# Performance work log

Measured on AMD Instinct MI355X. Metric: run time of the kernel, lower is better.

The kernel has to match this reference:

```python
import jax, jax.numpy as jnp
import numpy as np

CAP = 6.0
EPS = 1e-5

def _layernorm(x, g, b):
    mu = jnp.mean(x, axis=-1, keepdims=True)
    var = jnp.mean(jnp.square(x - mu), axis=-1, keepdims=True)
    return (x - mu) * jax.lax.rsqrt(var + EPS) * g + b

def setup_inputs() -> dict:
    key = jax.random.key(0)
    B, S, D, H = 4, 1024, 1024, 16
    DF = int(D * 2.0)
    ks = jax.random.split(key, 8)
    inp = {
        "x": jax.random.normal(ks[0], (B, S, D), dtype=jnp.float32),
        "mask": jnp.tril(jnp.ones((S, S), dtype=bool)),  # causal block mask
        "qkv_w": jax.random.normal(ks[1], (3 * D, D), dtype=jnp.float32) * 0.02,
        "qkv_b": jnp.zeros((3 * D,), dtype=jnp.float32),
        "out_w": jax.random.normal(ks[2], (D, D), dtype=jnp.float32) * 0.02,
        "out_b": jnp.zeros((D,), dtype=jnp.float32),
        "ln1_g": jnp.ones((D,), dtype=jnp.float32),
        "ln1_b": jnp.zeros((D,), dtype=jnp.float32),
        "ln2_g": jnp.ones((D,), dtype=jnp.float32),
        "ln2_b": jnp.zeros((D,), dtype=jnp.float32),
        "ff1_w": jax.random.normal(ks[3], (DF, D), dtype=jnp.float32) * 0.02,
        "ff1_b": jnp.zeros((DF,), dtype=jnp.float32),
        "ff2_w": jax.random.normal(ks[4], (D, DF), dtype=jnp.float32) * 0.02,
        "ff2_b": jnp.zeros((D,), dtype=jnp.float32),
    }
    return inp

def reference(x, mask, qkv_w, qkv_b, out_w, out_b, ln1_g, ln1_b, ln2_g, ln2_b,
              ff1_w, ff1_b, ff2_w, ff2_b):
    B, S, D = x.shape
    H = 16
    dh = D // H
    res = x
    h = _layernorm(x, ln1_g, ln1_b)
    qkv = h @ qkv_w.T + qkv_b                       # [B,S,3D]
    qkv = qkv.reshape(B, S, 3, H, dh).transpose(2, 0, 3, 1, 4)  # [3,B,H,S,dh]
    q, k, v = qkv[0], qkv[1], qkv[2]
    scores = jnp.einsum('bhqd,bhkd->bhqk', q, k) / jnp.sqrt(jnp.float32(dh))
    scores = CAP * jnp.tanh(scores / CAP)            # logit soft-cap score_mod
    scores = jnp.where(mask, scores, jnp.float32(-1e9))
    attn = jax.nn.softmax(scores, axis=-1)
    o = jnp.einsum('bhqk,bhkd->bhqd', attn, v)       # [B,H,S,dh]
    o = o.transpose(0, 2, 1, 3).reshape(B, S, D)
    x = res + (o @ out_w.T + out_b)
    h2 = _layernorm(x, ln2_g, ln2_b)
    ff = jax.nn.gelu(h2 @ ff1_w.T + ff1_b, approximate=False) @ ff2_w.T + ff2_b
    return x + ff
```

## Files before the change

kernel.cpp:

```cpp
#include <hip/hip_runtime.h>
#include <hip/hip_bf16.h>
#include <cmath>

#define NROWS 4096
#define DM    1024

typedef unsigned short u16;
typedef __attribute__((ext_vector_type(8))) short short8;
typedef __attribute__((ext_vector_type(4))) float floatx4;

#if __has_builtin(__builtin_amdgcn_exp2f)
#define EXP2F(x) __builtin_amdgcn_exp2f(x)
#else
#define EXP2F(x) exp2f(x)
#endif
#if __has_builtin(__builtin_amdgcn_rcpf)
#define RCPF(x) __builtin_amdgcn_rcpf(x)
#else
#define RCPF(x) (1.0f / (x))
#endif

__device__ __forceinline__ u16 f2bf(float f) {
    unsigned int u = __float_as_uint(f);
    return (u16)((u + 0x7fffu + ((u >> 16) & 1u)) >> 16);
}

__device__ __forceinline__ size_t pk_off(int row, int k, int KB) {
    const int rt = row >> 6, i = (row >> 4) & 3, lr = row & 15;
    const int kb = k >> 6, s = (k >> 5) & 1, lq = (k >> 3) & 3, j = k & 7;
    return ((((size_t)(rt * KB + kb) * 2 + s) * 4 + i) * 64 + lq * 16 + lr) * 8 + j;
}

__device__ __forceinline__ void async_copy16(const void* g, void* l) {
    __builtin_amdgcn_global_load_lds(
        (const __attribute__((address_space(1))) void*)g,
        (__attribute__((address_space(3))) void*)l, 16, 0, 0);
}

__global__ __launch_bounds__(256) void castln_kernel(
    const float* __restrict__ s0, const float* __restrict__ s1,
    const float* __restrict__ s2, const float* __restrict__ s3,
    u16* __restrict__ d0, u16* __restrict__ d1,
    u16* __restrict__ d2, u16* __restrict__ d3,
    const float* __restrict__ x, const float* __restrict__ g,
    const float* __restrict__ beta, u16* __restrict__ hout)
{
    const int bid = blockIdx.x;
    if (bid < 8192) {
        const float* s; u16* d; int base, kbits, KB;
        if (bid < 3072)      { s = s0; d = d0; base = bid;        kbits = 10; KB = 16; }
        else if (bid < 4096) { s = s1; d = d1; base = bid - 3072; kbits = 10; KB = 16; }
        else if (bid < 6144) { s = s2; d = d2; base = bid - 4096; kbits = 10; KB = 16; }
        else                 { s = s3; d = d3; base = bid - 6144; kbits = 11; KB = 32; }
        const int idx = (base * 256 + threadIdx.x) * 4;
        const float4 v = *(const float4*)(s + idx);
        const int row = idx >> kbits, k = idx & ((1 << kbits) - 1);
        *(ushort4*)(d + pk_off(row, k, KB)) =
            make_ushort4(f2bf(v.x), f2bf(v.y), f2bf(v.z), f2bf(v.w));
        return;
    }
    const int row = bid - 8192;
    const int t = threadIdx.x;
    const float4 v = ((const float4*)(x + (size_t)row * DM))[t];
    float s = v.x + v.y + v.z + v.w;
    #pragma unroll
    for (int off = 32; off > 0; off >>= 1) s += __shfl_xor(s, off);
    __shared__ float red[4];
    const int wid = t >> 6;
    if ((t & 63) == 0) red[wid] = s;
    __syncthreads();
    const float mean = (red[0] + red[1] + red[2] + red[3]) * (1.0f / DM);
    const float dx = v.x - mean, dy = v.y - mean, dz = v.z - mean, dw = v.w - mean;
    float ss = dx*dx + dy*dy + dz*dz + dw*dw;
    #pragma unroll
    for (int off = 32; off > 0; off >>= 1) ss += __shfl_xor(ss, off);
    __syncthreads();
    if ((t & 63) == 0) red[wid] = ss;
    __syncthreads();
    const float var = (red[0] + red[1] + red[2] + red[3]) * (1.0f / DM);
    const float rstd = rsqrtf(var + 1e-5f);
    const float4 gv = ((const float4*)g)[t];
    const float4 bv = ((const float4*)beta)[t];
    *(ushort4*)(hout + pk_off(row, t * 4, 16)) = make_ushort4(
        f2bf(dx * rstd * gv.x + bv.x), f2bf(dy * rstd * gv.y + bv.y),
        f2bf(dz * rstd * gv.z + bv.z), f2bf(dw * rstd * gv.w + bv.w));
}

__global__ __launch_bounds__(256) void ln_kernel(
    const float* __restrict__ x, const float* __restrict__ g,
    const float* __restrict__ beta, u16* __restrict__ out)
{
    const int row = blockIdx.x;
    const int t = threadIdx.x;
    const float4 v = ((const float4*)(x + (size_t)row * DM))[t];
    float s = v.x + v.y + v.z + v.w;
    #pragma unroll
    for (int off = 32; off > 0; off >>= 1) s += __shfl_xor(s, off);
    __shared__ float red[4];
    const int wid = t >> 6;
    if ((t & 63) == 0) red[wid] = s;
    __syncthreads();
    const float mean = (red[0] + red[1] + red[2] + red[3]) * (1.0f / DM);
    const float dx = v.x - mean, dy = v.y - mean, dz = v.z - mean, dw = v.w - mean;
    float ss = dx*dx + dy*dy + dz*dz + dw*dw;
    #pragma unroll
    for (int off = 32; off > 0; off >>= 1) ss += __shfl_xor(ss, off);
    __syncthreads();
    if ((t & 63) == 0) red[wid] = ss;
    __syncthreads();
    const float var = (red[0] + red[1] + red[2] + red[3]) * (1.0f / DM);
    const float rstd = rsqrtf(var + 1e-5f);
    const float4 gv = ((const float4*)g)[t];
    const float4 bv = ((const float4*)beta)[t];
    *(ushort4*)(out + pk_off(row, t * 4, 16)) = make_ushort4(
        f2bf(dx * rstd * gv.x + bv.x), f2bf(dy * rstd * gv.y + bv.y),
        f2bf(dz * rstd * gv.z + bv.z), f2bf(dw * rstd * gv.w + bv.w));
}

__device__ __forceinline__ float gelu_f(float v) {
    return 0.5f * v * (1.0f + erff(v * 0.70710678118654752f));
}

template <int ACT, int OUTMODE, int TM>
__global__ __launch_bounds__(256, TM == 128 ? 3 : 4) void gemm_pk_kernel(
    const u16* __restrict__ A, const u16* __restrict__ W,
    const float* __restrict__ bias, const float* __restrict__ res,
    void* __restrict__ Cout, u16* __restrict__ vtout, int N, int K)
{
    constexpr int MI = TM / 32;
    constexpr int SMEMB = (OUTMODE == 1) ? 34816 : 17408;
    __shared__ __align__(16) char smem[SMEMB];
    float* Cs = (float*)smem;

    const int tid = threadIdx.x;
    const int w = tid >> 6, l = tid & 63;
    const int lr = l & 15, lq = l >> 4;
    const int wm = w >> 1, wn = w & 1;

    const int fid = blockIdx.x;
    const int NB = (N >> 7) >> 3;
    const int xcd = fid & 7;
    const int kk = fid >> 3;
    constexpr int MT_BITS = (TM == 128) ? 5 : 6;
    constexpr int MT_MASK = (1 << MT_BITS) - 1;
    const int nt = xcd * NB + (kk >> MT_BITS);
    const int mt = kk & MT_MASK;
    const int m0 = mt * TM, n0 = nt * 128;
    const int KB = K >> 6;

    const int art = (TM == 128) ? (mt * 2 + wm) : mt;
    const u16* Ab = A + (size_t)art * KB * 4096 + l * 8;
    const u16* Wb = W + (size_t)(nt * 2 + wn) * KB * 4096 + l * 8;

    floatx4 acc[MI][4] = {};
    short8 a0[MI], b0[4], a1[MI], b1[4];
    #pragma unroll
    for (int i = 0; i < MI; i++) {
        const int fi = (TM == 128) ? i : (wm * 2 + i);
        a0[i] = *(const short8*)(Ab + fi * 512);
    }
    #pragma unroll
    for (int j = 0; j < 4; j++) b0[j] = *(const short8*)(Wb + j * 512);

    const int steps = K >> 5;
    for (int t = 0; t < steps; t += 2) {
        const u16* An = Ab + (size_t)(t + 1) * 2048;
        const u16* Wn = Wb + (size_t)(t + 1) * 2048;
        #pragma unroll
        for (int i = 0; i < MI; i++) {
            const int fi = (TM == 128) ? i : (wm * 2 + i);
            a1[i] = *(const short8*)(An + fi * 512);
        }
        #pragma unroll
        for (int j = 0; j < 4; j++) b1[j] = *(const short8*)(Wn + j * 512);
        #pragma unroll
        for (int i = 0; i < MI; i++)
            #pragma unroll
            for (int j = 0; j < 4; j++)
                acc[i][j] = __builtin_amdgcn_mfma_f32_16x16x32_bf16(a0[i], b0[j], acc[i][j], 0, 0, 0);
        if (t + 2 < steps) {
            const u16* An2 = Ab + (size_t)(t + 2) * 2048;
            const u16* Wn2 = Wb + (size_t)(t + 2) * 2048;
            #pragma unroll
            for (int i = 0; i < MI; i++) {
                const int fi = (TM == 128) ? i : (wm * 2 + i);
                a0[i] = *(const short8*)(An2 + fi * 512);
            }
            #pragma unroll
            for (int j = 0; j < 4; j++) b0[j] = *(const short8*)(Wn2 + j * 512);
        }
        #pragma unroll
        for (int i = 0; i < MI; i++)
            #pragma unroll
            for (int j = 0; j < 4; j++)
                acc[i][j] = __builtin_amdgcn_mfma_f32_16x16x32_bf16(a1[i], b1[j], acc[i][j], 0, 0, 0);
    }

    if (OUTMODE == 1 && n0 >= 2048) {
        short* Ts = (short*)smem;
        float bj[4];
        #pragma unroll
        for (int j = 0; j < 4; j++) bj[j] = bias[n0 + wn * 64 + j * 16 + lr];
        #pragma unroll
        for (int i = 0; i < 4; i++)
            #pragma unroll
            for (int j = 0; j < 4; j++) {
                const int vcol_l = wn * 64 + j * 16 + lr;
                const int sbase = wm * 64 + i * 16 + lq * 4;
                #pragma unroll
                for (int rp = 0; rp < 2; rp++) {
                    const unsigned pkv =
                        (unsigned)f2bf(acc[i][j][rp * 2] + bj[j]) |
                        ((unsigned)f2bf(acc[i][j][rp * 2 + 1] + bj[j]) << 16);
                    *(unsigned*)&Ts[vcol_l * 136 + sbase + rp * 2] = pkv;
                }
            }
        __syncthreads();
        const int bb = m0 >> 10, m0loc = m0 & 1023;
        const int R0 = bb * 1024 + (n0 - 2048);
        const int row = tid >> 1, p = tid & 1;
        u16* dst = vtout + (size_t)(R0 + row) * 1024 + m0loc + p * 64;
        const short* src = &Ts[row * 136 + p * 64];
        #pragma unroll
        for (int s = 0; s < 8; s++)
            *(short8*)(dst + s * 8) = *(const short8*)(src + s * 8);
        return;
    }

    #pragma unroll
    for (int i = 0; i < MI; i++) {
        __syncthreads();
        #pragma unroll
        for (int r = 0; r < 4; r++) {
            const int rl = wm * 16 + lq * 4 + r;
            #pragma unroll
            for (int j = 0; j < 4; j++)
                Cs[rl * 136 + wn * 64 + j * 16 + lr] = acc[i][j][r];
        }
        __syncthreads();
        #pragma unroll
        for (int q = 0; q < 2; q++) {
            const int s2 = tid * 2 + q;
            const int rid = s2 >> 4, c8 = s2 & 15;
            const int rr = m0 + (rid >> 4) * (TM / 2) + i * 16 + (rid & 15);
            const int col = c8 * 8;
            float vv[8];
            const float4 v0 = *(const float4*)&Cs[rid * 136 + col];
            const float4 v1 = *(const float4*)&Cs[rid * 136 + col + 4];
            const float4 ba = *(const float4*)&bias[n0 + col];
            const float4 bb4 = *(const float4*)&bias[n0 + col + 4];
            vv[0] = v0.x + ba.x;  vv[1] = v0.y + ba.y;  vv[2] = v0.z + ba.z;  vv[3] = v0.w + ba.w;
            vv[4] = v1.x + bb4.x; vv[5] = v1.y + bb4.y; vv[6] = v1.z + bb4.z; vv[7] = v1.w + bb4.w;
            if (ACT) {
                #pragma unroll
                for (int e = 0; e < 8; e++) vv[e] = gelu_f(vv[e]);
            }
            if (OUTMODE == 0) {
                const size_t o0 = (size_t)rr * N + n0 + col;
                if (res) {
                    const float4 r0 = *(const float4*)&res[o0];
                    const float4 r1 = *(const float4*)&res[o0 + 4];
                    vv[0]+=r0.x; vv[1]+=r0.y; vv[2]+=r0.z; vv[3]+=r0.w;
                    vv[4]+=r1.x; vv[5]+=r1.y; vv[6]+=r1.z; vv[7]+=r1.w;
                }
                *(float4*)((float*)Cout + o0)     = make_float4(vv[0], vv[1], vv[2], vv[3]);
                *(float4*)((float*)Cout + o0 + 4) = make_float4(vv[4], vv[5], vv[6], vv[7]);
            } else {
                short8 ov;
                #pragma unroll
                for (int e = 0; e < 8; e++) ov[e] = (short)f2bf(vv[e]);
                if (OUTMODE == 1)
                    *(short8*)((u16*)Cout + (size_t)rr * N + n0 + col) = ov;
                else
                    *(short8*)((u16*)Cout + pk_off(rr, n0 + col, N >> 6)) = ov;
            }
        }
    }
}

__global__ __launch_bounds__(256, 4) void attn_mfma_kernel(
    const u16* __restrict__ qkv,
    const u16* __restrict__ vt,
    u16* __restrict__ o)
{
    __shared__ __align__(16) short Ks[4096];
    __shared__ __align__(16) short Vs[4096];
    __shared__ __align__(16) short Ps[4][1152];

    const int qt = 15 - blockIdx.y;
    const int bh = blockIdx.x;
    const int b = bh >> 4, h = bh & 15;
    const int tid = threadIdx.x;
    const int w = tid >> 6, l = tid & 63;
    const int C = l & 15, Qd = l >> 4;

    const float C1f = 0.0601122935f, C2f = -17.3123404907f;

    short8 qf[2];
    {
        const u16* qp = qkv + (size_t)(b * 1024 + qt * 64 + w * 16 + C) * 3072 + h * 64 + Qd * 8;
        qf[0] = *(const short8*)qp;
        qf[1] = *(const short8*)(qp + 32);
    }

    const u16* kbase = qkv + (size_t)(b * 1024) * 3072 + 1024 + h * 64;
    const u16* vbase = vt + (size_t)(b * 16 + h) * 65536;

    float l_i = 0.f;
    floatx4 oacc[4] = {};

    for (int kt = 0; kt <= qt; kt++) {
        __syncthreads();
        #pragma unroll
        for (int ii = 0; ii < 4; ii++) {
            const int i = w * 4 + ii;
            if (i < 8) {
                const int mt = i >> 1, s = i & 1;
                async_copy16(kbase + (size_t)(kt * 64 + mt * 16 + C) * 3072 + s * 32 + Qd * 8,
                             &Ks[i * 512]);
            } else {
                const int j = i - 8, dt = j >> 1, s = j & 1;
                async_copy16(vbase + (size_t)(dt * 16 + C) * 1024 + kt * 64 + s * 32 + Qd * 8,
                             &Vs[j * 512]);
            }
        }
        __syncthreads();

        floatx4 sacc[4] = {};
        #pragma unroll
        for (int mt = 0; mt < 4; mt++)
            #pragma unroll
            for (int s = 0; s < 2; s++) {
                const short8 kf = *(const short8*)&Ks[((mt * 2 + s) * 64 + l) * 8];
                sacc[mt] = __builtin_amdgcn_mfma_f32_16x16x32_bf16(kf, qf[s], sacc[mt], 0, 0, 0);
            }

        float p[16];
        float rs = 0.f;
        const bool diag = (kt == qt);
        const int qrow = qt * 64 + w * 16 + C;
        #pragma unroll
        for (int mt = 0; mt < 4; mt++)
            #pragma unroll
            for (int r = 0; r < 4; r++) {
                const float e = EXP2F(sacc[mt][r] * C1f);
                float pv = EXP2F(C2f * RCPF(e + 1.0f));
                if (diag) {
                    const int krow = kt * 64 + mt * 16 + Qd * 4 + r;
                    if (krow > qrow) pv = 0.f;
                }
                p[mt * 4 + r] = pv;
                rs += pv;
            }
        rs += __shfl_xor(rs, 16);
        rs += __shfl_xor(rs, 32);
        l_i += rs;

        #pragma unroll
        for (int mt = 0; mt < 4; mt++)
            #pragma unroll
            for (int pr = 0; pr < 2; pr++) {
                union { __hip_bfloat162 b2; unsigned u; } cv;
                cv.b2 = __float22bfloat162_rn(
                    make_float2(p[mt * 4 + pr * 2], p[mt * 4 + pr * 2 + 1]));
                *(unsigned*)&Ps[w][C * 72 + mt * 16 + Qd * 4 + pr * 2] = cv.u;
            }
        short8 pf[2];
        pf[0] = *(const short8*)&Ps[w][C * 72 + Qd * 8];
        pf[1] = *(const short8*)&Ps[w][C * 72 + 32 + Qd * 8];

        #pragma unroll
        for (int dt = 0; dt < 4; dt++)
            #pragma unroll
            for (int s = 0; s < 2; s++) {
                const short8 vf = *(const short8*)&Vs[((dt * 2 + s) * 64 + l) * 8];
                oacc[dt] = __builtin_amdgcn_mfma_f32_16x16x32_bf16(pf[s], vf, oacc[dt], 0, 0, 0);
            }
    }

    float linv[4];
    #pragma unroll
    for (int r = 0; r < 4; r++) linv[r] = RCPF(__shfl(l_i, Qd * 4 + r));
    __syncthreads();
    #pragma unroll
    for (int dt = 0; dt < 4; dt++) {
        const int s = dt >> 1;
        const int lqp = (dt & 1) * 2 + (C >> 3);
        const int jj = C & 7;
        #pragma unroll
        for (int r = 0; r < 4; r++)
            Ks[((s * 4 + w) * 64 + lqp * 16 + Qd * 4 + r) * 8 + jj] =
                (short)f2bf(oacc[dt][r] * linv[r]);
    }
    __syncthreads();
    u16* obase = o + (size_t)((b * 16 + qt) * 16 + h) * 4096 + tid * 16;
    *(short8*)obase       = *(const short8*)&Ks[tid * 16];
    *(short8*)(obase + 8) = *(const short8*)&Ks[tid * 16 + 8];
}

extern "C" void kernel_launch(void* const* d_in, const int* in_sizes, int n_in,
                              void* d_out, int out_size, void* d_ws, size_t ws_size,
                              hipStream_t stream)
{
    (void)in_sizes; (void)n_in; (void)out_size; (void)ws_size;
    const float* x     = (const float*)d_in[0];
    const float* qkv_w = (const float*)d_in[2];
    const float* qkv_b = (const float*)d_in[3];
    const float* out_w = (const float*)d_in[4];
    const float* out_b = (const float*)d_in[5];
    const float* ln1_g = (const float*)d_in[6];
    const float* ln1_b = (const float*)d_in[7];
    const float* ln2_g = (const float*)d_in[8];
    const float* ln2_b = (const float*)d_in[9];
    const float* ff1_w = (const float*)d_in[10];
    const float* ff1_b = (const float*)d_in[11];
    const float* ff2_w = (const float*)d_in[12];
    const float* ff2_b = (const float*)d_in[13];
    float* out = (float*)d_out;

    u16* qkvbuf = (u16*)d_ws;
    u16* vtbuf  = (u16*)((char*)d_ws + 25165824);
    u16* hbuf   = (u16*)((char*)d_ws + 33554432);
    u16* obuf   = (u16*)((char*)d_ws + 41943040);
    u16* wq     = (u16*)((char*)d_ws + 50331648);
    u16* wo = wq + 3145728;
    u16* w1 = wo + 1048576;
    u16* w2 = w1 + 2097152;
    u16* ff1buf = qkvbuf;

    castln_kernel<<<12288, 256, 0, stream>>>(
        qkv_w, out_w, ff1_w, ff2_w, wq, wo, w1, w2, x, ln1_g, ln1_b, hbuf);
    gemm_pk_kernel<0,1,128><<<768, 256, 0, stream>>>(
        hbuf, wq, qkv_b, nullptr, qkvbuf, vtbuf, 3072, 1024);
    attn_mfma_kernel<<<dim3(64, 16), 256, 0, stream>>>(qkvbuf, vtbuf, obuf);
    gemm_pk_kernel<0,0,64><<<512, 256, 0, stream>>>(
        obuf, wo, out_b, x, out, nullptr, 1024, 1024);
    ln_kernel<<<NROWS, 256, 0, stream>>>(out, ln2_g, ln2_b, hbuf);
    gemm_pk_kernel<1,2,128><<<512, 256, 0, stream>>>(
        hbuf, w1, ff1_b, nullptr, ff1buf, nullptr, 2048, 1024);
    gemm_pk_kernel<0,0,64><<<512, 256, 0, stream>>>(
        ff1buf, w2, ff2_b, out, out, nullptr, 1024, 2048);
}
```

Measured before the change: 310.4 us.

## Emit Q/K/V in MFMA-fragment packed layout and load attention operands directly to registers

```diff
diff --git a/kernel.cpp b/kernel.cpp
--- a/kernel.cpp
+++ b/kernel.cpp
@@ -29,12 +29,6 @@
     const int rt = row >> 6, i = (row >> 4) & 3, lr = row & 15;
     const int kb = k >> 6, s = (k >> 5) & 1, lq = (k >> 3) & 3, j = k & 7;
     return ((((size_t)(rt * KB + kb) * 2 + s) * 4 + i) * 64 + lq * 16 + lr) * 8 + j;
-}
-
-__device__ __forceinline__ void async_copy16(const void* g, void* l) {
-    __builtin_amdgcn_global_load_lds(
-        (const __attribute__((address_space(1))) void*)g,
-        (__attribute__((address_space(3))) void*)l, 16, 0, 0);
 }
 
 __global__ __launch_bounds__(256) void castln_kernel(
@@ -125,7 +119,8 @@
 __global__ __launch_bounds__(256, TM == 128 ? 3 : 4) void gemm_pk_kernel(
     const u16* __restrict__ A, const u16* __restrict__ W,
     const float* __restrict__ bias, const float* __restrict__ res,
-    void* __restrict__ Cout, u16* __restrict__ vtout, int N, int K)
+    void* __restrict__ Cout, u16* __restrict__ vpout, u16* __restrict__ kpout,
+    int N, int K)
 {
     constexpr int MI = TM / 32;
     constexpr int SMEMB = (OUTMODE == 1) ? 34816 : 17408;
@@ -196,34 +191,68 @@
                 acc[i][j] = __builtin_amdgcn_mfma_f32_16x16x32_bf16(a1[i], b1[j], acc[i][j], 0, 0, 0);
     }
 
-    if (OUTMODE == 1 && n0 >= 2048) {
+    if (OUTMODE == 1) {
         short* Ts = (short*)smem;
         float bj[4];
         #pragma unroll
         for (int j = 0; j < 4; j++) bj[j] = bias[n0 + wn * 64 + j * 16 + lr];
-        #pragma unroll
-        for (int i = 0; i < 4; i++)
-            #pragma unroll
-            for (int j = 0; j < 4; j++) {
-                const int vcol_l = wn * 64 + j * 16 + lr;
-                const int sbase = wm * 64 + i * 16 + lq * 4;
+        const bool isV = (n0 >= 2048);
+        if (isV) {
+            #pragma unroll
+            for (int i = 0; i < 4; i++)
                 #pragma unroll
-                for (int rp = 0; rp < 2; rp++) {
-                    const unsigned pkv =
-                        (unsigned)f2bf(acc[i][j][rp * 2] + bj[j]) |
-                        ((unsigned)f2bf(acc[i][j][rp * 2 + 1] + bj[j]) << 16);
-                    *(unsigned*)&Ts[vcol_l * 136 + sbase + rp * 2] = pkv;
+                for (int j = 0; j < 4; j++) {
+                    const int vcol_l = wn * 64 + j * 16 + lr;
+                    const int sbase = wm * 64 + i * 16 + lq * 4;
+                    #pragma unroll
+                    for (int rp = 0; rp < 2; rp++) {
+                        const unsigned pkv =
+                            (unsigned)f2bf(acc[i][j][rp * 2] + bj[j]) |
+                            ((unsigned)f2bf(acc[i][j][rp * 2 + 1] + bj[j]) << 16);
+                        *(unsigned*)&Ts[vcol_l * 136 + sbase + rp * 2] = pkv;
+                    }
                 }
-            }
+        } else {
+            #pragma unroll
+            for (int i = 0; i < 4; i++)
+                #pragma unroll
+                for (int j = 0; j < 4; j++)
+                    #pragma unroll
+                    for (int r = 0; r < 4; r++) {
+                        const int row_l = wm * 64 + i * 16 + lq * 4 + r;
+                        const int col_l = wn * 64 + j * 16 + lr;
+                        Ts[row_l * 136 + col_l] = (short)f2bf(acc[i][j][r] + bj[j]);
+                    }
+        }
         __syncthreads();
-        const int bb = m0 >> 10, m0loc = m0 & 1023;
-        const int R0 = bb * 1024 + (n0 - 2048);
-        const int row = tid >> 1, p = tid & 1;
-        u16* dst = vtout + (size_t)(R0 + row) * 1024 + m0loc + p * 64;
-        const short* src = &Ts[row * 136 + p * 64];
-        #pragma unroll
-        for (int s = 0; s < 8; s++)
-            *(short8*)(dst + s * 8) = *(const short8*)(src + s * 8);
+        u16* dbuf = isV ? vpout : (n0 >= 1024 ? kpout : (u16*)Cout);
+        const int hbase = (n0 & 1023) >> 6;
+        const int l0 = (tid * 2) & 63, subp = tid >> 6, sp = (tid >> 5) & 1;
+        #pragma unroll
+        for (int tl = 0; tl < 2; tl++) {
+            const int mg = m0 + tl * 64;
+            const int bb2 = mg >> 10, ktile = (mg & 1023) >> 6;
+            #pragma unroll
+            for (int hl = 0; hl < 2; hl++) {
+                const int hh = hbase + hl;
+                u16* dst = dbuf + ((size_t)(bb2 * 16 + hh) * 16 + ktile) * 4096 + tid * 16;
+                #pragma unroll
+                for (int half = 0; half < 2; half++) {
+                    const int ll = l0 + half;
+                    short8 seg;
+                    if (isV) {
+                        const int vcol_l = hl * 64 + subp * 16 + (ll & 15);
+                        const int srow = tl * 64 + sp * 32 + ((ll >> 4) & 3) * 8;
+                        seg = *(const short8*)&Ts[vcol_l * 136 + srow];
+                    } else {
+                        const int row_l = tl * 64 + subp * 16 + (ll & 15);
+                        const int col_l = hl * 64 + sp * 32 + ((ll >> 4) & 3) * 8;
+                        seg = *(const short8*)&Ts[row_l * 136 + col_l];
+                    }
+                    *(short8*)(dst + half * 8) = seg;
+                }
+            }
+        }
         return;
     }
 
@@ -269,23 +298,18 @@
                 short8 ov;
                 #pragma unroll
                 for (int e = 0; e < 8; e++) ov[e] = (short)f2bf(vv[e]);
-                if (OUTMODE == 1)
-                    *(short8*)((u16*)Cout + (size_t)rr * N + n0 + col) = ov;
-                else
-                    *(short8*)((u16*)Cout + pk_off(rr, n0 + col, N >> 6)) = ov;
-            }
-        }
-    }
-}
-
-__global__ __launch_bounds__(256, 4) void attn_mfma_kernel(
-    const u16* __restrict__ qkv,
-    const u16* __restrict__ vt,
-    u16* __restrict__ o)
+                *(short8*)((u16*)Cout + pk_off(rr, n0 + col, N >> 6)) = ov;
+            }
+        }
+    }
+}
+
+__global__ __launch_bounds__(256, 3) void attn_mfma_kernel(
+    const u16* __restrict__ qp, const u16* __restrict__ kp,
+    const u16* __restrict__ vp, u16* __restrict__ o)
 {
-    __shared__ __align__(16) short Ks[4096];
-    __shared__ __align__(16) short Vs[4096];
     __shared__ __align__(16) short Ps[4][1152];
+    __shared__ __align__(16) short Os[4096];
 
     const int qt = 15 - blockIdx.y;
     const int bh = blockIdx.x;
@@ -296,44 +320,40 @@
 
     const float C1f = 0.0601122935f, C2f = -17.3123404907f;
 
+    const size_t headoff = (size_t)(b * 16 + h) * 16 * 4096;
+    const u16* qb = qp + headoff + (size_t)qt * 4096 + w * 1024 + l * 8;
+    const u16* kb = kp + headoff + l * 8;
+    const u16* vb = vp + headoff + l * 8;
+
     short8 qf[2];
-    {
-        const u16* qp = qkv + (size_t)(b * 1024 + qt * 64 + w * 16 + C) * 3072 + h * 64 + Qd * 8;
-        qf[0] = *(const short8*)qp;
-        qf[1] = *(const short8*)(qp + 32);
-    }
-
-    const u16* kbase = qkv + (size_t)(b * 1024) * 3072 + 1024 + h * 64;
-    const u16* vbase = vt + (size_t)(b * 16 + h) * 65536;
+    qf[0] = *(const short8*)qb;
+    qf[1] = *(const short8*)(qb + 512);
 
     float l_i = 0.f;
     floatx4 oacc[4] = {};
 
+    short8 kf[8];
+    #pragma unroll
+    for (int i = 0; i < 8; i++) kf[i] = *(const short8*)(kb + i * 512);
+
     for (int kt = 0; kt <= qt; kt++) {
-        __syncthreads();
-        #pragma unroll
-        for (int ii = 0; ii < 4; ii++) {
-            const int i = w * 4 + ii;
-            if (i < 8) {
-                const int mt = i >> 1, s = i & 1;
-                async_copy16(kbase + (size_t)(kt * 64 + mt * 16 + C) * 3072 + s * 32 + Qd * 8,
-                             &Ks[i * 512]);
-            } else {
-                const int j = i - 8, dt = j >> 1, s = j & 1;
-                async_copy16(vbase + (size_t)(dt * 16 + C) * 1024 + kt * 64 + s * 32 + Qd * 8,
-                             &Vs[j * 512]);
-            }
-        }
-        __syncthreads();
+        const u16* vv_ = vb + (size_t)kt * 4096;
+        short8 vf[8];
+        #pragma unroll
+        for (int j = 0; j < 8; j++) vf[j] = *(const short8*)(vv_ + j * 512);
 
         floatx4 sacc[4] = {};
         #pragma unroll
         for (int mt = 0; mt < 4; mt++)
             #pragma unroll
-            for (int s = 0; s < 2; s++) {
-                const short8 kf = *(const short8*)&Ks[((mt * 2 + s) * 64 + l) * 8];
-                sacc[mt] = __builtin_amdgcn_mfma_f32_16x16x32_bf16(kf, qf[s], sacc[mt], 0, 0, 0);
-            }
+            for (int s = 0; s < 2; s++)
+                sacc[mt] = __builtin_amdgcn_mfma_f32_16x16x32_bf16(kf[mt * 2 + s], qf[s], sacc[mt], 0, 0, 0);
+
+        if (kt < qt) {
+            const u16* kn_ = kb + (size_t)(kt + 1) * 4096;
+            #pragma unroll
+            for (int i = 0; i < 8; i++) kf[i] = *(const short8*)(kn_ + i * 512);
+        }
 
         float p[16];
         float rs = 0.f;
@@ -372,16 +392,13 @@
         #pragma unroll
         for (int dt = 0; dt < 4; dt++)
             #pragma unroll
-            for (int s = 0; s < 2; s++) {
-                const short8 vf = *(const short8*)&Vs[((dt * 2 + s) * 64 + l) * 8];
-                oacc[dt] = __builtin_amdgcn_mfma_f32_16x16x32_bf16(pf[s], vf, oacc[dt], 0, 0, 0);
-            }
+            for (int s = 0; s < 2; s++)
+                oacc[dt] = __builtin_amdgcn_mfma_f32_16x16x32_bf16(pf[s], vf[dt * 2 + s], oacc[dt], 0, 0, 0);
     }
 
     float linv[4];
     #pragma unroll
     for (int r = 0; r < 4; r++) linv[r] = RCPF(__shfl(l_i, Qd * 4 + r));
-    __syncthreads();
     #pragma unroll
     for (int dt = 0; dt < 4; dt++) {
         const int s = dt >> 1;
@@ -389,13 +406,13 @@
         const int jj = C & 7;
         #pragma unroll
         for (int r = 0; r < 4; r++)
-            Ks[((s * 4 + w) * 64 + lqp * 16 + Qd * 4 + r) * 8 + jj] =
+            Os[((s * 4 + w) * 64 + lqp * 16 + Qd * 4 + r) * 8 + jj] =
                 (short)f2bf(oacc[dt][r] * linv[r]);
     }
     __syncthreads();
     u16* obase = o + (size_t)((b * 16 + qt) * 16 + h) * 4096 + tid * 16;
-    *(short8*)obase       = *(const short8*)&Ks[tid * 16];
-    *(short8*)(obase + 8) = *(const short8*)&Ks[tid * 16 + 8];
+    *(short8*)obase       = *(const short8*)&Os[tid * 16];
+    *(short8*)(obase + 8) = *(const short8*)&Os[tid * 16 + 8];
 }
 
 extern "C" void kernel_launch(void* const* d_in, const int* in_sizes, int n_in,
@@ -418,26 +435,27 @@
     const float* ff2_b = (const float*)d_in[13];
     float* out = (float*)d_out;
 
-    u16* qkvbuf = (u16*)d_ws;
-    u16* vtbuf  = (u16*)((char*)d_ws + 25165824);
-    u16* hbuf   = (u16*)((char*)d_ws + 33554432);
-    u16* obuf   = (u16*)((char*)d_ws + 41943040);
-    u16* wq     = (u16*)((char*)d_ws + 50331648);
+    u16* qpbuf = (u16*)d_ws;
+    u16* kpbuf = qpbuf + 4194304;
+    u16* vpbuf = kpbuf + 4194304;
+    u16* hbuf  = (u16*)((char*)d_ws + 33554432);
+    u16* obuf  = (u16*)((char*)d_ws + 41943040);
+    u16* wq    = (u16*)((char*)d_ws + 50331648);
     u16* wo = wq + 3145728;
     u16* w1 = wo + 1048576;
     u16* w2 = w1 + 2097152;
-    u16* ff1buf = qkvbuf;
+    u16* ff1buf = (u16*)d_ws;
 
     castln_kernel<<<12288, 256, 0, stream>>>(
         qkv_w, out_w, ff1_w, ff2_w, wq, wo, w1, w2, x, ln1_g, ln1_b, hbuf);
     gemm_pk_kernel<0,1,128><<<768, 256, 0, stream>>>(
-        hbuf, wq, qkv_b, nullptr, qkvbuf, vtbuf, 3072, 1024);
-    attn_mfma_kernel<<<dim3(64, 16), 256, 0, stream>>>(qkvbuf, vtbuf, obuf);
+        hbuf, wq, qkv_b, nullptr, qpbuf, vpbuf, kpbuf, 3072, 1024);
+    attn_mfma_kernel<<<dim3(64, 16), 256, 0, stream>>>(qpbuf, kpbuf, vpbuf, obuf);
     gemm_pk_kernel<0,0,64><<<512, 256, 0, stream>>>(
-        obuf, wo, out_b, x, out, nullptr, 1024, 1024);
+        obuf, wo, out_b, x, out, nullptr, nullptr, 1024, 1024);
     ln_kernel<<<NROWS, 256, 0, stream>>>(out, ln2_g, ln2_b, hbuf);
     gemm_pk_kernel<1,2,128><<<512, 256, 0, stream>>>(
-        hbuf, w1, ff1_b, nullptr, ff1buf, nullptr, 2048, 1024);
+        hbuf, w1, ff1_b, nullptr, ff1buf, nullptr, nullptr, 2048, 1024);
     gemm_pk_kernel<0,0,64><<<512, 256, 0, stream>>>(
-        ff1buf, w2, ff2_b, out, out, nullptr, 1024, 2048);
-}
+        ff1buf, w2, ff2_b, out, out, nullptr, nullptr, 1024, 2048);
+}
```

New measurement: 294.9 us. 5.0% less time.
